# Performance work log

Hardware: AMD Instinct MI355X
Metric: run time of the kernel (lower is better)

The kernel has to match this reference:

```python
import jax, jax.numpy as jnp
import numpy as np

DIM = 768
HEADS = 12
HD = DIM // HEADS  # 64
BASE = 100.0


def rope_sincos(H, W):
    # DINOv3 RopePositionEmbedding: normalize_coords='separate', base=100.0
    dd = HD // 4
    periods = BASE ** (jnp.arange(dd, dtype=jnp.float32) / dd)          # [dd]
    ch = (jnp.arange(H, dtype=jnp.float32) + 0.5) / H                    # pixel centers
    cw = (jnp.arange(W, dtype=jnp.float32) + 0.5) / W
    cy, cx = jnp.meshgrid(ch, cw, indexing='ij')
    coords = 2.0 * jnp.stack([cy, cx], axis=-1).reshape(H * W, 2) - 1.0  # [N,2] in [-1,1]
    angles = 2.0 * jnp.pi * coords[:, :, None] / periods[None, None, :]  # [N,2,dd]
    angles = angles.reshape(H * W, 2 * dd)                               # [N, HD//2]
    angles = jnp.concatenate([angles, angles], axis=-1)                  # [N, HD]
    return jnp.sin(angles), jnp.cos(angles)


def rotate_half(t):
    t1, t2 = jnp.split(t, 2, axis=-1)
    return jnp.concatenate([-t2, t1], axis=-1)


def setup_inputs() -> dict:
    key = jax.random.key(0)
    k1, k2, k3 = jax.random.split(key, 3)
    B, H, W = 2, 48, 48
    x = jax.random.normal(k1, (B, H, W, DIM), dtype=jnp.float32)
    w_qkv = jax.random.normal(k2, (3 * DIM, DIM), dtype=jnp.float32) * 0.02
    b_qkv = jnp.zeros((3 * DIM,), dtype=jnp.float32)
    w_proj = jax.random.normal(k3, (DIM, DIM), dtype=jnp.float32) * 0.02
    b_proj = jnp.zeros((DIM,), dtype=jnp.float32)
    return {"x": x, "w_qkv": w_qkv, "b_qkv": b_qkv, "w_proj": w_proj, "b_proj": b_proj}


def reference(x, w_qkv, b_qkv, w_proj, b_proj):
    B, H, W, C = x.shape
    N = H * W
    xf = x.reshape(B, N, C)
    qkv = xf @ w_qkv.T + b_qkv                                   # [B,N,3C]
    qkv = qkv.reshape(B, N, 3, HEADS, HD).transpose(2, 0, 3, 1, 4)
    q, k, v = qkv[0], qkv[1], qkv[2]                              # [B,h,N,d]
    sin, cos = rope_sincos(H, W)                                  # [N,d]
    q = q * cos + rotate_half(q) * sin
    k = k * cos + rotate_half(k) * sin
    scale = HD ** -0.5
    attn = jax.nn.softmax(jnp.einsum('bhqd,bhkd->bhqk', q, k) * scale, axis=-1)
    o = jnp.einsum('bhqk,bhkd->bhqd', attn, v)                    # [B,h,N,d]
    o = o.transpose(0, 2, 1, 3).reshape(B, N, C)
    o = o @ w_proj.T + b_proj
    return o.reshape(B, H, W, C)
```

## Files before the change

kernel.cpp:

```cpp
#include <hip/hip_runtime.h>

#define BATCH 2
#define NSEQ 2304
#define DIM 768
#define HEADS 12
#define HD 64
#define M_TOK (BATCH * NSEQ)
#define LDSP 72
#define KP 72
#define BH (BATCH * HEADS)
#define KT_HALF (NSEQ / 64 / 2)

typedef __attribute__((ext_vector_type(8))) short bf16x8;
typedef __attribute__((ext_vector_type(8))) short short8v;
typedef __attribute__((ext_vector_type(4))) float f32x4;
typedef _Float16 half4 __attribute__((ext_vector_type(4)));
typedef _Float16 half8 __attribute__((ext_vector_type(8)));

#define QSCALE (0.125f * 1.44269504088896f)
#define LOG2_100_D16 0.41524101186092029f

__device__ __forceinline__ short f2bf(float f) {
    union { float f; unsigned u; } v; v.f = f;
    unsigned r = v.u + 0x7fffu + ((v.u >> 16) & 1u);
    return (short)(r >> 16);
}
__device__ __forceinline__ float bf2f(short s) {
    union { unsigned u; float f; } v; v.u = ((unsigned)(unsigned short)s) << 16;
    return v.f;
}

#define CN1 (M_TOK * DIM / 4)
#define CN2 (3 * DIM * DIM / 4)
#define CN3 (DIM * DIM / 4)
__global__ void cvt_all_kernel(const float* __restrict__ x, const float* __restrict__ wq,
                               const float* __restrict__ wp,
                               short* __restrict__ xb, short* __restrict__ wqb,
                               short* __restrict__ wpb) {
    int i = blockIdx.x * 256 + threadIdx.x;
    const float* src; short* dst; int j;
    if (i < CN1)              { src = x;  dst = xb;  j = i; }
    else if (i < CN1 + CN2)   { src = wq; dst = wqb; j = i - CN1; }
    else                      { src = wp; dst = wpb; j = i - CN1 - CN2; }
    float4 v = reinterpret_cast<const float4*>(src)[j];
    short4 o;
    o.x = f2bf(v.x); o.y = f2bf(v.y); o.z = f2bf(v.z); o.w = f2bf(v.w);
    reinterpret_cast<short4*>(dst)[j] = o;
}

__global__ __launch_bounds__(256) void gemm_qkv_kernel(
    const short* __restrict__ A,
    const short* __restrict__ Bt,
    const float* __restrict__ bias,
    short* __restrict__ qb, short* __restrict__ kbuf, _Float16* __restrict__ vtb)
{
    __shared__ __align__(16) short At[128 * LDSP];
    __shared__ __align__(16) short Bl[128 * LDSP];
    const int m0 = blockIdx.x * 128, n0 = blockIdx.y * 128;
    const int tid = threadIdx.x, lane = tid & 63, wave = tid >> 6;
    const int quad = lane >> 4, l16 = lane & 15;
    const int wm = (wave >> 1) * 64, wn = (wave & 1) * 64;
    const int r = tid >> 1, c0 = (tid & 1) * 32;
    f32x4 acc[4][4] = {};

    for (int k0 = 0; k0 < DIM; k0 += 64) {
        const uint4* ga = reinterpret_cast<const uint4*>(&A[(size_t)(m0 + r) * DIM + k0 + c0]);
        const uint4* gb = reinterpret_cast<const uint4*>(&Bt[(size_t)(n0 + r) * DIM + k0 + c0]);
        uint4 a0 = ga[0], a1 = ga[1], a2 = ga[2], a3 = ga[3];
        uint4 b0 = gb[0], b1 = gb[1], b2 = gb[2], b3 = gb[3];
        uint4* sa = reinterpret_cast<uint4*>(&At[r * LDSP + c0]);
        uint4* sb = reinterpret_cast<uint4*>(&Bl[r * LDSP + c0]);
        sa[0] = a0; sa[1] = a1; sa[2] = a2; sa[3] = a3;
        sb[0] = b0; sb[1] = b1; sb[2] = b2; sb[3] = b3;
        __syncthreads();
#pragma unroll
        for (int ks = 0; ks < 2; ++ks) {
            bf16x8 af[4], bf[4];
#pragma unroll
            for (int mt = 0; mt < 4; ++mt)
                af[mt] = *reinterpret_cast<const bf16x8*>(&At[(wm + mt * 16 + l16) * LDSP + ks * 32 + quad * 8]);
#pragma unroll
            for (int nt = 0; nt < 4; ++nt)
                bf[nt] = *reinterpret_cast<const bf16x8*>(&Bl[(wn + nt * 16 + l16) * LDSP + ks * 32 + quad * 8]);
#pragma unroll
            for (int mt = 0; mt < 4; ++mt)
#pragma unroll
                for (int nt = 0; nt < 4; ++nt)
                    acc[mt][nt] = __builtin_amdgcn_mfma_f32_16x16x32_bf16(af[mt], bf[nt], acc[mt][nt], 0, 0, 0);
        }
        __syncthreads();
    }

    const int which = (n0 + wn) / DIM;
    const int head = ((n0 + wn) % DIM) / HD;
    const int b = m0 / NSEQ;
    const int tokb = m0 % NSEQ + wm;
    if (which == 2) {
#pragma unroll
        for (int mt = 0; mt < 4; ++mt)
#pragma unroll
            for (int nt = 0; nt < 4; ++nt) {
                const int n = n0 + wn + nt * 16 + l16;
                const int d = nt * 16 + l16;
                const float bi = bias[n];
                const int tok0 = tokb + mt * 16 + quad * 4;
                half4 hv;
                hv.x = (_Float16)(acc[mt][nt][0] + bi);
                hv.y = (_Float16)(acc[mt][nt][1] + bi);
                hv.z = (_Float16)(acc[mt][nt][2] + bi);
                hv.w = (_Float16)(acc[mt][nt][3] + bi);
                *reinterpret_cast<half4*>(&vtb[((size_t)(b * HEADS + head) * HD + d) * NSEQ + tok0]) = hv;
            }
    } else {
        short* dst = (which == 0) ? qb : kbuf;
        const float qs = (which == 0) ? QSCALE : 1.0f;
        float bi[4];
#pragma unroll
        for (int nt = 0; nt < 4; ++nt) bi[nt] = bias[n0 + wn + nt * 16 + l16];
        const float invp = __builtin_amdgcn_exp2f(-(float)l16 * LOG2_100_D16);
#pragma unroll
        for (int mt = 0; mt < 4; ++mt) {
#pragma unroll
            for (int rg = 0; rg < 4; ++rg) {
                const int tok = tokb + mt * 16 + quad * 4 + rg;
                const int yy = tok / 48, xx = tok - yy * 48;
                const float ry = (2.0f * (yy + 0.5f) * (1.0f / 48.0f) - 1.0f) * invp;
                const float rx = (2.0f * (xx + 0.5f) * (1.0f / 48.0f) - 1.0f) * invp;
                const float sy = __builtin_amdgcn_sinf(ry), cy = __builtin_amdgcn_cosf(ry);
                const float sx = __builtin_amdgcn_sinf(rx), cx = __builtin_amdgcn_cosf(rx);
                const float a0 = acc[mt][0][rg] + bi[0];
                const float a1 = acc[mt][1][rg] + bi[1];
                const float a2 = acc[mt][2][rg] + bi[2];
                const float a3 = acc[mt][3][rg] + bi[3];
                short* rp = &dst[((size_t)(b * HEADS + head) * NSEQ + tok) * HD];
                rp[l16]      = f2bf((a0 * cy - a2 * sy) * qs);
                rp[32 + l16] = f2bf((a2 * cy + a0 * sy) * qs);
                rp[16 + l16] = f2bf((a1 * cx - a3 * sx) * qs);
                rp[48 + l16] = f2bf((a3 * cx + a1 * sx) * qs);
            }
        }
    }
}

__global__ __launch_bounds__(256) void attn_kernel(
    const short* __restrict__ qb, const short* __restrict__ kb,
    const _Float16* __restrict__ vtb, _Float16* __restrict__ opart,
    float* __restrict__ lpart)
{
    __shared__ __align__(16) short    Kt[2][64 * KP];
    __shared__ __align__(16) _Float16 Vt[2][64 * KP];
    const int qt = blockIdx.x, kh = blockIdx.y, bh = blockIdx.z;
    const int tid = threadIdx.x, lane = tid & 63, wave = tid >> 6;
    const int quad = lane >> 4, l16 = lane & 15;
    const int qrow0 = qt * 128 + wave * 32;
    const short* qbase = qb + (size_t)bh * NSEQ * HD;
    const short* kbase = kb + (size_t)bh * NSEQ * HD;
    const _Float16* vbase = vtb + (size_t)bh * HD * NSEQ;

    bf16x8 qf[2][2];
#pragma unroll
    for (int mt = 0; mt < 2; ++mt)
#pragma unroll
        for (int ks = 0; ks < 2; ++ks)
            qf[mt][ks] = *reinterpret_cast<const bf16x8*>(
                &qbase[(size_t)(qrow0 + mt * 16 + l16) * HD + ks * 32 + quad * 8]);

    half4 ones;
    ones.x = ones.y = ones.z = ones.w = (_Float16)1.0f;

    f32x4 oacc[2][4] = {};
    f32x4 lacc[2] = {};

    const int r = tid >> 2, cq = (tid & 3) * 16;
    const int t0 = kh * KT_HALF;
    {
        const uint4* gk = reinterpret_cast<const uint4*>(&kbase[(size_t)(t0 * 64 + r) * HD + cq]);
        uint4 k0 = gk[0], k1 = gk[1];
        const uint4* gv = reinterpret_cast<const uint4*>(&vbase[(size_t)r * NSEQ + t0 * 64 + cq]);
        uint4 v0 = gv[0], v1 = gv[1];
        uint4* sk = reinterpret_cast<uint4*>(&Kt[0][r * KP + cq]);
        sk[0] = k0; sk[1] = k1;
        uint4* sv = reinterpret_cast<uint4*>(&Vt[0][r * KP + cq]);
        sv[0] = v0; sv[1] = v1;
    }

    int cur = 0;
    for (int kt = 0; kt < KT_HALF; ++kt) {
        uint4 k0, k1, v0, v1;
        if (kt + 1 < KT_HALF) {
            const int nb0 = (t0 + kt + 1) * 64;
            const uint4* gk = reinterpret_cast<const uint4*>(&kbase[(size_t)(nb0 + r) * HD + cq]);
            k0 = gk[0]; k1 = gk[1];
            const uint4* gv = reinterpret_cast<const uint4*>(&vbase[(size_t)r * NSEQ + nb0 + cq]);
            v0 = gv[0]; v1 = gv[1];
        }
        __syncthreads();

        f32x4 sacc[4][2] = {};
#pragma unroll
        for (int ks = 0; ks < 2; ++ks) {
#pragma unroll
            for (int nt = 0; nt < 4; ++nt) {
                bf16x8 kf = *reinterpret_cast<const bf16x8*>(
                    &Kt[cur][(nt * 16 + l16) * KP + ks * 32 + quad * 8]);
#pragma unroll
                for (int mt = 0; mt < 2; ++mt)
                    sacc[nt][mt] = __builtin_amdgcn_mfma_f32_16x16x32_bf16(
                        kf, qf[mt][ks], sacc[nt][mt], 0, 0, 0);
            }
        }

        half4 pf[2][4];
#pragma unroll
        for (int mt = 0; mt < 2; ++mt)
#pragma unroll
            for (int nt = 0; nt < 4; ++nt) {
                pf[mt][nt].x = (_Float16)__builtin_amdgcn_exp2f(sacc[nt][mt][0]);
                pf[mt][nt].y = (_Float16)__builtin_amdgcn_exp2f(sacc[nt][mt][1]);
                pf[mt][nt].z = (_Float16)__builtin_amdgcn_exp2f(sacc[nt][mt][2]);
                pf[mt][nt].w = (_Float16)__builtin_amdgcn_exp2f(sacc[nt][mt][3]);
            }

#pragma unroll
        for (int mt = 0; mt < 2; ++mt)
#pragma unroll
            for (int nt = 0; nt < 4; ++nt)
                lacc[mt] = __builtin_amdgcn_mfma_f32_16x16x16f16(
                    pf[mt][nt], ones, lacc[mt], 0, 0, 0);

#pragma unroll
        for (int nt = 0; nt < 4; ++nt)
#pragma unroll
            for (int dt = 0; dt < 4; ++dt) {
                half4 vf = *reinterpret_cast<const half4*>(
                    &Vt[cur][(dt * 16 + l16) * KP + nt * 16 + quad * 4]);
#pragma unroll
                for (int mt = 0; mt < 2; ++mt)
                    oacc[mt][dt] = __builtin_amdgcn_mfma_f32_16x16x16f16(
                        pf[mt][nt], vf, oacc[mt][dt], 0, 0, 0);
            }

        if (kt + 1 < KT_HALF) {
            uint4* sk = reinterpret_cast<uint4*>(&Kt[cur ^ 1][r * KP + cq]);
            sk[0] = k0; sk[1] = k1;
            uint4* sv = reinterpret_cast<uint4*>(&Vt[cur ^ 1][r * KP + cq]);
            sv[0] = v0; sv[1] = v1;
        }
        cur ^= 1;
    }

    _Float16* ob2 = opart + (size_t)(kh * BH + bh) * NSEQ * HD;
    float* lp2 = lpart + (size_t)(kh * BH + bh) * NSEQ;
#pragma unroll
    for (int mt = 0; mt < 2; ++mt) {
#pragma unroll
        for (int dt = 0; dt < 4; ++dt)
#pragma unroll
            for (int rg = 0; rg < 4; ++rg) {
                int row = qrow0 + mt * 16 + quad * 4 + rg;
                ob2[(size_t)row * HD + dt * 16 + l16] = (_Float16)oacc[mt][dt][rg];
            }
        if (l16 == 0) {
#pragma unroll
            for (int rg = 0; rg < 4; ++rg)
                lp2[qrow0 + mt * 16 + quad * 4 + rg] = lacc[mt][rg];
        }
    }
}

__global__ __launch_bounds__(256) void gemm_proj_kernel(
    const _Float16* __restrict__ op,
    const float* __restrict__ lp,
    const short* __restrict__ Bt,
    const float* __restrict__ bias,
    float* __restrict__ out)
{
    __shared__ __align__(16) short At[64 * LDSP];
    __shared__ __align__(16) short Bl[64 * LDSP];
    const int m0 = blockIdx.x * 64, n0 = blockIdx.y * 64;
    const int tid = threadIdx.x, lane = tid & 63, wave = tid >> 6;
    const int quad = lane >> 4, l16 = lane & 15;
    const int wm = (wave >> 1) * 32, wn = (wave & 1) * 32;
    const int r = tid >> 2, cs = (tid & 3) * 16;
    const int b = m0 / NSEQ;
    const int tok = m0 % NSEQ + r;
    f32x4 acc[2][2] = {};

    for (int k0 = 0; k0 < DIM; k0 += 64) {
        const int h = k0 >> 6;
        const size_t pb = (size_t)(b * HEADS + h) * NSEQ + tok;
        const float l0 = lp[pb], l1 = lp[(size_t)BH * NSEQ + pb];
        const float inv = __builtin_amdgcn_rcpf(l0 + l1);
        const half8* o0 = reinterpret_cast<const half8*>(&op[pb * HD + cs]);
        const half8* o1 = reinterpret_cast<const half8*>(&op[(size_t)BH * NSEQ * HD + pb * HD + cs]);
        half8 p0 = o0[0], p1 = o0[1], q0 = o1[0], q1 = o1[1];
        const uint4* gb = reinterpret_cast<const uint4*>(&Bt[(size_t)(n0 + r) * DIM + k0 + cs]);
        uint4 bw0 = gb[0], bw1 = gb[1];
        short8v s0, s1;
#pragma unroll
        for (int j = 0; j < 8; ++j) {
            s0[j] = f2bf(((float)p0[j] + (float)q0[j]) * inv);
            s1[j] = f2bf(((float)p1[j] + (float)q1[j]) * inv);
        }
        *reinterpret_cast<short8v*>(&At[r * LDSP + cs]) = s0;
        *reinterpret_cast<short8v*>(&At[r * LDSP + cs + 8]) = s1;
        uint4* sb = reinterpret_cast<uint4*>(&Bl[r * LDSP + cs]);
        sb[0] = bw0; sb[1] = bw1;
        __syncthreads();
#pragma unroll
        for (int ks = 0; ks < 2; ++ks) {
            bf16x8 af[2], bf[2];
#pragma unroll
            for (int mt = 0; mt < 2; ++mt)
                af[mt] = *reinterpret_cast<const bf16x8*>(&At[(wm + mt * 16 + l16) * LDSP + ks * 32 + quad * 8]);
#pragma unroll
            for (int nt = 0; nt < 2; ++nt)
                bf[nt] = *reinterpret_cast<const bf16x8*>(&Bl[(wn + nt * 16 + l16) * LDSP + ks * 32 + quad * 8]);
#pragma unroll
            for (int mt = 0; mt < 2; ++mt)
#pragma unroll
                for (int nt = 0; nt < 2; ++nt)
                    acc[mt][nt] = __builtin_amdgcn_mfma_f32_16x16x32_bf16(af[mt], bf[nt], acc[mt][nt], 0, 0, 0);
        }
        __syncthreads();
    }

#pragma unroll
    for (int mt = 0; mt < 2; ++mt)
#pragma unroll
        for (int nt = 0; nt < 2; ++nt) {
            const int n = n0 + wn + nt * 16 + l16;
            const float bi = bias[n];
#pragma unroll
            for (int rg = 0; rg < 4; ++rg) {
                const int m = m0 + wm + mt * 16 + quad * 4 + rg;
                out[(size_t)m * DIM + n] = acc[mt][nt][rg] + bi;
            }
        }
}

extern "C" void kernel_launch(void* const* d_in, const int* in_sizes, int n_in,
                              void* d_out, int out_size, void* d_ws, size_t ws_size,
                              hipStream_t stream) {
    const float* x      = (const float*)d_in[0];
    const float* w_qkv  = (const float*)d_in[1];
    const float* b_qkv  = (const float*)d_in[2];
    const float* w_proj = (const float*)d_in[3];
    const float* b_proj = (const float*)d_in[4];
    float* out = (float*)d_out;

    short* xb     = (short*)d_ws;
    short* wqkvb  = xb + (size_t)M_TOK * DIM;
    short* wprojb = wqkvb + (size_t)3 * DIM * DIM;
    short* qb     = wprojb + (size_t)DIM * DIM;
    short* kb     = qb + (size_t)BH * NSEQ * HD;
    short* vtb    = kb + (size_t)BH * NSEQ * HD;
    short* opart  = vtb + (size_t)BH * NSEQ * HD;
    float* lpart  = (float*)(opart + (size_t)2 * BH * NSEQ * HD);

    cvt_all_kernel<<<(CN1 + CN2 + CN3) / 256, 256, 0, stream>>>(
        x, w_qkv, w_proj, xb, wqkvb, wprojb);

    dim3 g1(M_TOK / 128, 3 * DIM / 128);
    gemm_qkv_kernel<<<g1, 256, 0, stream>>>(xb, wqkvb, b_qkv, qb, kb, (_Float16*)vtb);

    dim3 g2(NSEQ / 128, 2, BH);
    attn_kernel<<<g2, 256, 0, stream>>>(qb, kb, (const _Float16*)vtb,
                                        (_Float16*)opart, lpart);

    dim3 g3(M_TOK / 64, DIM / 64);
    gemm_proj_kernel<<<g3, 256, 0, stream>>>((const _Float16*)opart, lpart,
                                             wprojb, b_proj, out);
}
```

Before: 184.9 us.

## Double-buffer QKV GEMM LDS tiles and use packed fp16 conversion in attention

The QKV GEMM now keeps two LDS buffers for the A and B tiles. It prefetches the next K-slice from global memory into registers while MFMAs run on the current buffer, then writes that slice into the other buffer, so only one barrier per iteration is needed. In the attention kernel the barrier moves to the top of the loop, and the four exp2 results are converted to fp16 in pairs with cvt_pkrtz, which rounds toward zero. The double buffering doubles LDS use in the GEMM, which may lower occupancy, and the round-toward-zero conversion changes numerics slightly.

```diff
diff --git a/kernel.cpp b/kernel.cpp
--- a/kernel.cpp
+++ b/kernel.cpp
@@ -14,6 +14,7 @@
 typedef __attribute__((ext_vector_type(8))) short bf16x8;
 typedef __attribute__((ext_vector_type(8))) short short8v;
 typedef __attribute__((ext_vector_type(4))) float f32x4;
+typedef __fp16 fp16x2 __attribute__((ext_vector_type(2)));
 typedef _Float16 half4 __attribute__((ext_vector_type(4)));
 typedef _Float16 half8 __attribute__((ext_vector_type(8)));
 
@@ -24,10 +25,6 @@
     union { float f; unsigned u; } v; v.f = f;
     unsigned r = v.u + 0x7fffu + ((v.u >> 16) & 1u);
     return (short)(r >> 16);
-}
-__device__ __forceinline__ float bf2f(short s) {
-    union { unsigned u; float f; } v; v.u = ((unsigned)(unsigned short)s) << 16;
-    return v.f;
 }
 
 #define CN1 (M_TOK * DIM / 4)
@@ -54,8 +51,8 @@
     const float* __restrict__ bias,
     short* __restrict__ qb, short* __restrict__ kbuf, _Float16* __restrict__ vtb)
 {
-    __shared__ __align__(16) short At[128 * LDSP];
-    __shared__ __align__(16) short Bl[128 * LDSP];
+    __shared__ __align__(16) short At[2][128 * LDSP];
+    __shared__ __align__(16) short Bl[2][128 * LDSP];
     const int m0 = blockIdx.x * 128, n0 = blockIdx.y * 128;
     const int tid = threadIdx.x, lane = tid & 63, wave = tid >> 6;
     const int quad = lane >> 4, l16 = lane & 15;
@@ -63,32 +60,50 @@
     const int r = tid >> 1, c0 = (tid & 1) * 32;
     f32x4 acc[4][4] = {};
 
-    for (int k0 = 0; k0 < DIM; k0 += 64) {
-        const uint4* ga = reinterpret_cast<const uint4*>(&A[(size_t)(m0 + r) * DIM + k0 + c0]);
-        const uint4* gb = reinterpret_cast<const uint4*>(&Bt[(size_t)(n0 + r) * DIM + k0 + c0]);
+    {
+        const uint4* ga = reinterpret_cast<const uint4*>(&A[(size_t)(m0 + r) * DIM + c0]);
+        const uint4* gb = reinterpret_cast<const uint4*>(&Bt[(size_t)(n0 + r) * DIM + c0]);
         uint4 a0 = ga[0], a1 = ga[1], a2 = ga[2], a3 = ga[3];
         uint4 b0 = gb[0], b1 = gb[1], b2 = gb[2], b3 = gb[3];
-        uint4* sa = reinterpret_cast<uint4*>(&At[r * LDSP + c0]);
-        uint4* sb = reinterpret_cast<uint4*>(&Bl[r * LDSP + c0]);
+        uint4* sa = reinterpret_cast<uint4*>(&At[0][r * LDSP + c0]);
+        uint4* sb = reinterpret_cast<uint4*>(&Bl[0][r * LDSP + c0]);
         sa[0] = a0; sa[1] = a1; sa[2] = a2; sa[3] = a3;
         sb[0] = b0; sb[1] = b1; sb[2] = b2; sb[3] = b3;
+    }
+
+    int cur = 0;
+    for (int k0 = 0; k0 < DIM; k0 += 64) {
         __syncthreads();
+        uint4 a0, a1, a2, a3, b0, b1, b2, b3;
+        const bool pre = (k0 + 64 < DIM);
+        if (pre) {
+            const uint4* ga = reinterpret_cast<const uint4*>(&A[(size_t)(m0 + r) * DIM + k0 + 64 + c0]);
+            const uint4* gb = reinterpret_cast<const uint4*>(&Bt[(size_t)(n0 + r) * DIM + k0 + 64 + c0]);
+            a0 = ga[0]; a1 = ga[1]; a2 = ga[2]; a3 = ga[3];
+            b0 = gb[0]; b1 = gb[1]; b2 = gb[2]; b3 = gb[3];
+        }
 #pragma unroll
         for (int ks = 0; ks < 2; ++ks) {
             bf16x8 af[4], bf[4];
 #pragma unroll
             for (int mt = 0; mt < 4; ++mt)
-                af[mt] = *reinterpret_cast<const bf16x8*>(&At[(wm + mt * 16 + l16) * LDSP + ks * 32 + quad * 8]);
+                af[mt] = *reinterpret_cast<const bf16x8*>(&At[cur][(wm + mt * 16 + l16) * LDSP + ks * 32 + quad * 8]);
 #pragma unroll
             for (int nt = 0; nt < 4; ++nt)
-                bf[nt] = *reinterpret_cast<const bf16x8*>(&Bl[(wn + nt * 16 + l16) * LDSP + ks * 32 + quad * 8]);
+                bf[nt] = *reinterpret_cast<const bf16x8*>(&Bl[cur][(wn + nt * 16 + l16) * LDSP + ks * 32 + quad * 8]);
 #pragma unroll
             for (int mt = 0; mt < 4; ++mt)
 #pragma unroll
                 for (int nt = 0; nt < 4; ++nt)
                     acc[mt][nt] = __builtin_amdgcn_mfma_f32_16x16x32_bf16(af[mt], bf[nt], acc[mt][nt], 0, 0, 0);
         }
-        __syncthreads();
+        if (pre) {
+            uint4* sa = reinterpret_cast<uint4*>(&At[cur ^ 1][r * LDSP + c0]);
+            uint4* sb = reinterpret_cast<uint4*>(&Bl[cur ^ 1][r * LDSP + c0]);
+            sa[0] = a0; sa[1] = a1; sa[2] = a2; sa[3] = a3;
+            sb[0] = b0; sb[1] = b1; sb[2] = b2; sb[3] = b3;
+        }
+        cur ^= 1;
     }
 
     const int which = (n0 + wn) / DIM;
@@ -186,15 +201,16 @@
 
     int cur = 0;
     for (int kt = 0; kt < KT_HALF; ++kt) {
+        __syncthreads();
         uint4 k0, k1, v0, v1;
-        if (kt + 1 < KT_HALF) {
+        const bool pre = (kt + 1 < KT_HALF);
+        if (pre) {
             const int nb0 = (t0 + kt + 1) * 64;
             const uint4* gk = reinterpret_cast<const uint4*>(&kbase[(size_t)(nb0 + r) * HD + cq]);
             k0 = gk[0]; k1 = gk[1];
             const uint4* gv = reinterpret_cast<const uint4*>(&vbase[(size_t)r * NSEQ + nb0 + cq]);
             v0 = gv[0]; v1 = gv[1];
         }
-        __syncthreads();
 
         f32x4 sacc[4][2] = {};
 #pragma unroll
@@ -215,10 +231,16 @@
         for (int mt = 0; mt < 2; ++mt)
 #pragma unroll
             for (int nt = 0; nt < 4; ++nt) {
-                pf[mt][nt].x = (_Float16)__builtin_amdgcn_exp2f(sacc[nt][mt][0]);
-                pf[mt][nt].y = (_Float16)__builtin_amdgcn_exp2f(sacc[nt][mt][1]);
-                pf[mt][nt].z = (_Float16)__builtin_amdgcn_exp2f(sacc[nt][mt][2]);
-                pf[mt][nt].w = (_Float16)__builtin_amdgcn_exp2f(sacc[nt][mt][3]);
+                fp16x2 lo = __builtin_amdgcn_cvt_pkrtz(
+                    __builtin_amdgcn_exp2f(sacc[nt][mt][0]),
+                    __builtin_amdgcn_exp2f(sacc[nt][mt][1]));
+                fp16x2 hi = __builtin_amdgcn_cvt_pkrtz(
+                    __builtin_amdgcn_exp2f(sacc[nt][mt][2]),
+                    __builtin_amdgcn_exp2f(sacc[nt][mt][3]));
+                half4 p;
+                p.x = (_Float16)lo.x; p.y = (_Float16)lo.y;
+                p.z = (_Float16)hi.x; p.w = (_Float16)hi.y;
+                pf[mt][nt] = p;
             }
 
 #pragma unroll
@@ -240,7 +262,7 @@
                         pf[mt][nt], vf, oacc[mt][dt], 0, 0, 0);
             }
 
-        if (kt + 1 < KT_HALF) {
+        if (pre) {
             uint4* sk = reinterpret_cast<uint4*>(&Kt[cur ^ 1][r * KP + cq]);
             sk[0] = k0; sk[1] = k1;
             uint4* sv = reinterpret_cast<uint4*>(&Vt[cur ^ 1][r * KP + cq]);
```

Result: slower. 190.5 us (+3.0%).
